# Optimization experiments

Hardware: AMD Instinct MI355X
Metric: run time of the kernel (lower is better)

The kernel has to match this reference:

```python
import jax, jax.numpy as jnp
import numpy as np

B, N, DIM = 2, 2048, 2048
H, KVH, HD = 16, 4, 128
N_REP = H // KVH
SCALE = np.float32(HD ** -0.5)


def setup_inputs() -> dict:
    key = jax.random.key(0)
    ks = jax.random.split(key, 5)
    x = jax.random.normal(ks[0], (B, N, DIM), dtype=jnp.float32)
    mask = jnp.tril(jnp.ones((N, N), dtype=jnp.int32))[None, None]  # [1,1,N,N] causal
    Wq = jax.random.normal(ks[1], (DIM, H * HD), dtype=jnp.float32) * (DIM ** -0.5)
    Wk = jax.random.normal(ks[2], (DIM, KVH * HD), dtype=jnp.float32) * (DIM ** -0.5)
    Wv = jax.random.normal(ks[3], (DIM, KVH * HD), dtype=jnp.float32) * (DIM ** -0.5)
    Wo = jax.random.normal(ks[4], (H * HD, DIM), dtype=jnp.float32) * ((H * HD) ** -0.5)
    return {"x": x, "mask": mask, "Wq": Wq, "Wk": Wk, "Wv": Wv, "Wo": Wo}


def reference(x, mask, Wq, Wk, Wv, Wo):
    Bx, Nx, _ = x.shape
    # projections -> [B, heads, N, head_dim]
    q = (x @ Wq).reshape(Bx, Nx, H, HD).transpose(0, 2, 1, 3)
    k = (x @ Wk).reshape(Bx, Nx, KVH, HD).transpose(0, 2, 1, 3)
    v = (x @ Wv).reshape(Bx, Nx, KVH, HD).transpose(0, 2, 1, 3)
    # repeat_interleave KV heads to match query heads (GQA)
    k = jnp.repeat(k, N_REP, axis=1)
    v = jnp.repeat(v, N_REP, axis=1)
    attn = jnp.einsum('bhqd,bhkd->bhqk', q, k) * SCALE
    attn = jnp.where(mask == 0, jnp.float32(-jnp.inf), attn)
    attn = jax.nn.softmax(attn, axis=-1)
    out = jnp.einsum('bhqk,bhkd->bhqd', attn, v)
    out = out.transpose(0, 2, 1, 3).reshape(Bx, Nx, H * HD)
    return out @ Wo
```

## Files before the change

kernel.cpp:

```cpp
#include <hip/hip_runtime.h>
#include <hip/hip_bf16.h>
#include <math.h>

typedef __bf16 bf16;
typedef bf16 bf16x8 __attribute__((ext_vector_type(8)));
typedef bf16 bf16x4v __attribute__((ext_vector_type(4)));
typedef float f32x4 __attribute__((ext_vector_type(4)));

#define GLD16(g, l) __builtin_amdgcn_global_load_lds(                          \
    (__attribute__((address_space(1))) void*)(g),                              \
    (__attribute__((address_space(3))) void*)(l), 16, 0, 0)

#define MFMA16(a, b, c) __builtin_amdgcn_mfma_f32_16x16x32_bf16((a), (b), (c), 0, 0, 0)

#if __has_builtin(__builtin_amdgcn_exp2f)
#define EXP2F(x) __builtin_amdgcn_exp2f(x)
#else
#define EXP2F(x) exp2f(x)
#endif

__device__ __forceinline__ f32x4 shfl_xor4(f32x4 a, int m) {
  f32x4 r;
  #pragma unroll
  for (int i = 0; i < 4; i++) r[i] = __shfl_xor(a[i], m);
  return r;
}

__global__ void cast_f32_bf16(const float* __restrict__ in, bf16* __restrict__ out, int n4) {
  int i = blockIdx.x * blockDim.x + threadIdx.x;
  if (i < n4) {
    float4 v = ((const float4*)in)[i];
    bf16x4v o;
    o.x = (bf16)v.x; o.y = (bf16)v.y; o.z = (bf16)v.z; o.w = (bf16)v.w;
    ((bf16x4v*)out)[i] = o;
  }
}

__global__ void transpose_cast(const float* __restrict__ in, bf16* __restrict__ out,
                               int colsIn, int outStride, int outRowOff, float scale) {
  __shared__ float t[32][33];
  int c0 = blockIdx.x * 32, r0 = blockIdx.y * 32;
  int tx = threadIdx.x, ty = threadIdx.y;
  #pragma unroll
  for (int i = 0; i < 32; i += 8)
    t[ty + i][tx] = in[(size_t)(r0 + ty + i) * colsIn + (c0 + tx)];
  __syncthreads();
  #pragma unroll
  for (int i = 0; i < 32; i += 8)
    out[(size_t)(outRowOff + c0 + ty + i) * outStride + (r0 + tx)] = (bf16)(t[tx][ty + i] * scale);
}

__global__ void transpose_v(const bf16* __restrict__ QKV, bf16* __restrict__ Vg) {
  __shared__ bf16 t[32][34];
  int n0 = blockIdx.x * 32, d0 = blockIdx.y * 32;
  int bk = blockIdx.z;
  int b = bk >> 2, kvh = bk & 3;
  const bf16* src = QKV + (size_t)b * 2048 * 3072 + 2560 + kvh * 128;
  bf16* dst = Vg + (size_t)bk * 128 * 2048;
  int tx = threadIdx.x, ty = threadIdx.y;
  #pragma unroll
  for (int i = 0; i < 32; i += 8)
    t[ty + i][tx] = src[(size_t)(n0 + ty + i) * 3072 + (d0 + tx)];
  __syncthreads();
  #pragma unroll
  for (int i = 0; i < 32; i += 8)
    dst[(size_t)(d0 + ty + i) * 2048 + (n0 + tx)] = t[tx][ty + i];
}

template <typename OutT>
__global__ __launch_bounds__(256, 2) void gemm_bt(const bf16* __restrict__ A,
                                                  const bf16* __restrict__ Bt,
                                                  OutT* __restrict__ C,
                                                  int M, int N, int K) {
  __shared__ __attribute__((aligned(16))) bf16 As[128 * 32];
  __shared__ __attribute__((aligned(16))) bf16 Bs[128 * 32];
  const int tid = threadIdx.x;
  const int lane = tid & 63;
  const int wave = tid >> 6;
  const int wm = wave >> 1, wn = wave & 1;
  const int l15 = lane & 15, quad = lane >> 4;
  const int rowBase = blockIdx.y * 128;
  const int colBase = blockIdx.x * 128;

  f32x4 acc[4][4] = {};

  const int cb0 = wave * 64;
  const int c0 = cb0 + lane;
  const int c1 = c0 + 256;
  const bf16* a0 = A + (size_t)(rowBase + (c0 >> 2)) * K + (c0 & 3) * 8;
  const bf16* a1 = A + (size_t)(rowBase + (c1 >> 2)) * K + (c1 & 3) * 8;
  const bf16* b0 = Bt + (size_t)(colBase + (c0 >> 2)) * K + (c0 & 3) * 8;
  const bf16* b1 = Bt + (size_t)(colBase + (c1 >> 2)) * K + (c1 & 3) * 8;
  bf16* lA0 = &As[cb0 * 8];
  bf16* lA1 = &As[(cb0 + 256) * 8];
  bf16* lB0 = &Bs[cb0 * 8];
  bf16* lB1 = &Bs[(cb0 + 256) * 8];

  for (int k0 = 0; k0 < K; k0 += 32) {
    GLD16(a0 + k0, lA0);
    GLD16(a1 + k0, lA1);
    GLD16(b0 + k0, lB0);
    GLD16(b1 + k0, lB1);
    __syncthreads();
    bf16x8 af[4], bfr[4];
    #pragma unroll
    for (int i = 0; i < 4; i++)
      af[i] = *(const bf16x8*)&As[(wm * 64 + i * 16 + l15) * 32 + quad * 8];
    #pragma unroll
    for (int i = 0; i < 4; i++)
      bfr[i] = *(const bf16x8*)&Bs[(wn * 64 + i * 16 + l15) * 32 + quad * 8];
    #pragma unroll
    for (int i = 0; i < 4; i++)
      #pragma unroll
      for (int j = 0; j < 4; j++)
        acc[i][j] = MFMA16(af[i], bfr[j], acc[i][j]);
    __syncthreads();
  }

  #pragma unroll
  for (int i = 0; i < 4; i++) {
    int row = rowBase + wm * 64 + i * 16 + quad * 4;
    #pragma unroll
    for (int j = 0; j < 4; j++) {
      int col = colBase + wn * 64 + j * 16 + l15;
      #pragma unroll
      for (int r = 0; r < 4; r++)
        C[(size_t)(row + r) * N + col] = (OutT)acc[i][j][r];
    }
  }
}

#define MASKV (-1e30f)

__global__ __launch_bounds__(256, 2) void gqa_attn(const bf16* __restrict__ QKV,
                                                   const bf16* __restrict__ Vg,
                                                   bf16* __restrict__ Obf) {
  __shared__ __attribute__((aligned(16))) bf16 Kl[64 * 128];
  __shared__ __attribute__((aligned(16))) bf16 Vt[128 * 64];
  __shared__ __attribute__((aligned(16))) bf16 Pl[4][32 * 68];

  const int tid = threadIdx.x;
  const int lane = tid & 63;
  const int wave = tid >> 6;
  const int l15 = lane & 15, quad = lane >> 4;

  int bi = blockIdx.x;
  int bh = bi & 31;
  int jj = (bi & 255) >> 5;
  int qt = (bi < 256) ? (8 + jj) : (7 - jj);
  int b = bh >> 4, h = bh & 15, kvh = h >> 2;
  int q0 = qt * 128;

  const size_t rs = 3072;
  const bf16* Qb  = QKV + (size_t)b * 2048 * rs + h * 128;
  const bf16* Kb  = QKV + (size_t)b * 2048 * rs + 2048 + kvh * 128;
  const bf16* Vgb = Vg + (size_t)(b * 4 + kvh) * 128 * 2048;

  bf16x8 qf[2][4];
  #pragma unroll
  for (int mt = 0; mt < 2; mt++) {
    int row = q0 + wave * 32 + mt * 16 + l15;
    #pragma unroll
    for (int ks = 0; ks < 4; ks++)
      qf[mt][ks] = *(const bf16x8*)&Qb[(size_t)row * rs + ks * 32 + quad * 8];
  }

  const bf16* kp[4]; const bf16* vp[4];
  bf16* kl[4]; bf16* vl[4];
  #pragma unroll
  for (int t = 0; t < 4; t++) {
    int keyl = wave * 16 + t * 4 + (lane >> 4);
    int ck = (lane & 15) ^ (4 * (t & 1) + (lane >> 4));
    kp[t] = Kb + (size_t)keyl * rs + ck * 8;
    kl[t] = &Kl[(wave * 16 + t * 4) * 128];
    int dl = wave * 32 + t * 8 + (lane >> 3);
    int cv = (lane & 7) ^ (lane >> 3);
    vp[t] = Vgb + (size_t)dl * 2048 + cv * 8;
    vl[t] = &Vt[(wave * 32 + t * 8) * 64];
  }

  f32x4 oacc[2][8] = {};
  f32x4 mrow[2], lrow[2];
  #pragma unroll
  for (int mt = 0; mt < 2; mt++)
    #pragma unroll
    for (int r = 0; r < 4; r++) { mrow[mt][r] = MASKV; lrow[mt][r] = 0.f; }

  const int nkt = 2 * qt + 2;
  const int myrow_hi = q0 + wave * 32 + 31;
  for (int kt = 0; kt < nkt; kt++) {
    const int k0 = kt * 64;
    __syncthreads();
    #pragma unroll
    for (int t = 0; t < 4; t++) { GLD16(kp[t], kl[t]); kp[t] += 64 * rs; }
    #pragma unroll
    for (int t = 0; t < 4; t++) { GLD16(vp[t], vl[t]); vp[t] += 64; }
    __syncthreads();

    if (k0 > myrow_hi) continue;

    f32x4 s[2][4] = {};
    #pragma unroll
    for (int ks = 0; ks < 4; ks++) {
      #pragma unroll
      for (int nt = 0; nt < 4; nt++) {
        bf16x8 kf = *(const bf16x8*)&Kl[(nt * 16 + l15) * 128 +
                                        (((ks * 4 + quad) ^ (l15 & 7)) * 8)];
        s[0][nt] = MFMA16(qf[0][ks], kf, s[0][nt]);
        s[1][nt] = MFMA16(qf[1][ks], kf, s[1][nt]);
      }
    }
    if (kt >= nkt - 2) {
      #pragma unroll
      for (int mt = 0; mt < 2; mt++) {
        int rowb = q0 + wave * 32 + mt * 16 + quad * 4;
        #pragma unroll
        for (int nt = 0; nt < 4; nt++) {
          int col = k0 + nt * 16 + l15;
          #pragma unroll
          for (int r = 0; r < 4; r++)
            if (col > rowb + r) s[mt][nt][r] = MASKV;
        }
      }
    }
    #pragma unroll
    for (int mt = 0; mt < 2; mt++) {
      f32x4 mx = s[mt][0];
      #pragma unroll
      for (int nt = 1; nt < 4; nt++)
        #pragma unroll
        for (int r = 0; r < 4; r++) mx[r] = fmaxf(mx[r], s[mt][nt][r]);
      #pragma unroll
      for (int d = 1; d < 16; d <<= 1) {
        f32x4 o = shfl_xor4(mx, d);
        #pragma unroll
        for (int r = 0; r < 4; r++) mx[r] = fmaxf(mx[r], o[r]);
      }
      f32x4 mnew, alpha;
      #pragma unroll
      for (int r = 0; r < 4; r++) {
        mnew[r] = fmaxf(mrow[mt][r], mx[r]);
        alpha[r] = EXP2F(mrow[mt][r] - mnew[r]);
      }
      f32x4 rsum = {0.f, 0.f, 0.f, 0.f};
      #pragma unroll
      for (int nt = 0; nt < 4; nt++)
        #pragma unroll
        for (int r = 0; r < 4; r++) {
          float p = EXP2F(s[mt][nt][r] - mnew[r]);
          s[mt][nt][r] = p;
          rsum[r] += p;
        }
      #pragma unroll
      for (int d = 1; d < 16; d <<= 1) rsum += shfl_xor4(rsum, d);
      #pragma unroll
      for (int r = 0; r < 4; r++) {
        lrow[mt][r] = lrow[mt][r] * alpha[r] + rsum[r];
        mrow[mt][r] = mnew[r];
      }
      #pragma unroll
      for (int no = 0; no < 8; no++)
        #pragma unroll
        for (int r = 0; r < 4; r++) oacc[mt][no][r] *= alpha[r];
      #pragma unroll
      for (int nt = 0; nt < 4; nt++)
        #pragma unroll
        for (int r = 0; r < 4; r++)
          Pl[wave][(mt * 16 + quad * 4 + r) * 68 + nt * 16 + l15] = (bf16)s[mt][nt][r];
    }
    #pragma unroll
    for (int ks2 = 0; ks2 < 2; ks2++) {
      bf16x8 pf0 = *(const bf16x8*)&Pl[wave][l15 * 68 + ks2 * 32 + quad * 8];
      bf16x8 pf1 = *(const bf16x8*)&Pl[wave][(16 + l15) * 68 + ks2 * 32 + quad * 8];
      #pragma unroll
      for (int no = 0; no < 8; no++) {
        bf16x8 vf = *(const bf16x8*)&Vt[(no * 16 + l15) * 64 +
                                        (((ks2 * 4 + quad) ^ (l15 & 7)) * 8)];
        oacc[0][no] = MFMA16(pf0, vf, oacc[0][no]);
        oacc[1][no] = MFMA16(pf1, vf, oacc[1][no]);
      }
    }
  }

  #pragma unroll
  for (int mt = 0; mt < 2; mt++) {
    f32x4 linv;
    #pragma unroll
    for (int r = 0; r < 4; r++) linv[r] = 1.0f / lrow[mt][r];
    int row = q0 + wave * 32 + mt * 16 + quad * 4;
    #pragma unroll
    for (int no = 0; no < 8; no++) {
      int col = h * 128 + no * 16 + l15;
      #pragma unroll
      for (int r = 0; r < 4; r++)
        Obf[(size_t)(b * 2048 + row + r) * 2048 + col] = (bf16)(oacc[mt][no][r] * linv[r]);
    }
  }
}

extern "C" void kernel_launch(void* const* d_in, const int* in_sizes, int n_in,
                              void* d_out, int out_size, void* d_ws, size_t ws_size,
                              hipStream_t stream) {
  const float* x  = (const float*)d_in[0];
  const float* Wq = (const float*)d_in[2];
  const float* Wk = (const float*)d_in[3];
  const float* Wv = (const float*)d_in[4];
  const float* Wo = (const float*)d_in[5];
  float* out = (float*)d_out;

  bf16* Xb    = (bf16*)d_ws;
  bf16* Wqkvt = Xb + 8388608;
  bf16* Wot   = Wqkvt + 6291456;
  bf16* QKV   = Wot + 4194304;
  bf16* Obf   = QKV + 12582912;
  bf16* Vg    = Obf + 8388608;

  const float qscale = (float)(0.08838834764831845 * 1.4426950408889634);

  cast_f32_bf16<<<8192, 256, 0, stream>>>(x, Xb, 2097152);
  dim3 tb(32, 8);
  transpose_cast<<<dim3(64, 64), tb, 0, stream>>>(Wq, Wqkvt, 2048, 2048, 0, qscale);
  transpose_cast<<<dim3(16, 64), tb, 0, stream>>>(Wk, Wqkvt, 512, 2048, 2048, 1.0f);
  transpose_cast<<<dim3(16, 64), tb, 0, stream>>>(Wv, Wqkvt, 512, 2048, 2560, 1.0f);
  transpose_cast<<<dim3(64, 64), tb, 0, stream>>>(Wo, Wot, 2048, 2048, 0, 1.0f);

  gemm_bt<bf16><<<dim3(24, 32), 256, 0, stream>>>(Xb, Wqkvt, QKV, 4096, 3072, 2048);
  transpose_v<<<dim3(64, 4, 8), tb, 0, stream>>>(QKV, Vg);
  gqa_attn<<<512, 256, 0, stream>>>(QKV, Vg, Obf);
  gemm_bt<float><<<dim3(16, 32), 256, 0, stream>>>(Obf, Wot, out, 4096, 2048, 2048);
}
```

Baseline: 339.2 us.

## Double-buffer K/V tiles in LDS and prefetch next tile during compute

After: 349.8 us. 3.1% more time.

```diff
diff --git a/kernel.cpp b/kernel.cpp
--- a/kernel.cpp
+++ b/kernel.cpp
@@ -135,9 +135,9 @@
 __global__ __launch_bounds__(256, 2) void gqa_attn(const bf16* __restrict__ QKV,
                                                    const bf16* __restrict__ Vg,
                                                    bf16* __restrict__ Obf) {
-  __shared__ __attribute__((aligned(16))) bf16 Kl[64 * 128];
-  __shared__ __attribute__((aligned(16))) bf16 Vt[128 * 64];
-  __shared__ __attribute__((aligned(16))) bf16 Pl[4][32 * 68];
+  __shared__ __attribute__((aligned(16))) bf16 Kl[2 * 64 * 128];
+  __shared__ __attribute__((aligned(16))) bf16 Vt[2 * 128 * 64];
+  __shared__ __attribute__((aligned(16))) bf16 Pl[4][16 * 72];
 
   const int tid = threadIdx.x;
   const int lane = tid & 63;
@@ -166,17 +166,17 @@
   }
 
   const bf16* kp[4]; const bf16* vp[4];
-  bf16* kl[4]; bf16* vl[4];
+  int klo[4], vlo[4];
   #pragma unroll
   for (int t = 0; t < 4; t++) {
     int keyl = wave * 16 + t * 4 + (lane >> 4);
     int ck = (lane & 15) ^ (4 * (t & 1) + (lane >> 4));
     kp[t] = Kb + (size_t)keyl * rs + ck * 8;
-    kl[t] = &Kl[(wave * 16 + t * 4) * 128];
+    klo[t] = (wave * 16 + t * 4) * 128;
     int dl = wave * 32 + t * 8 + (lane >> 3);
     int cv = (lane & 7) ^ (lane >> 3);
     vp[t] = Vgb + (size_t)dl * 2048 + cv * 8;
-    vl[t] = &Vt[(wave * 32 + t * 8) * 64];
+    vlo[t] = (wave * 32 + t * 8) * 64;
   }
 
   f32x4 oacc[2][8] = {};
@@ -188,98 +188,119 @@
 
   const int nkt = 2 * qt + 2;
   const int myrow_hi = q0 + wave * 32 + 31;
+
+  #pragma unroll
+  for (int t = 0; t < 4; t++) { GLD16(kp[t], Kl + klo[t]); kp[t] += 64 * rs; }
+  #pragma unroll
+  for (int t = 0; t < 4; t++) { GLD16(vp[t], Vt + vlo[t]); vp[t] += 64; }
+  __syncthreads();
+
   for (int kt = 0; kt < nkt; kt++) {
+    const int cur = kt & 1;
     const int k0 = kt * 64;
-    __syncthreads();
-    #pragma unroll
-    for (int t = 0; t < 4; t++) { GLD16(kp[t], kl[t]); kp[t] += 64 * rs; }
-    #pragma unroll
-    for (int t = 0; t < 4; t++) { GLD16(vp[t], vl[t]); vp[t] += 64; }
-    __syncthreads();
-
-    if (k0 > myrow_hi) continue;
-
-    f32x4 s[2][4] = {};
-    #pragma unroll
-    for (int ks = 0; ks < 4; ks++) {
-      #pragma unroll
-      for (int nt = 0; nt < 4; nt++) {
-        bf16x8 kf = *(const bf16x8*)&Kl[(nt * 16 + l15) * 128 +
-                                        (((ks * 4 + quad) ^ (l15 & 7)) * 8)];
-        s[0][nt] = MFMA16(qf[0][ks], kf, s[0][nt]);
-        s[1][nt] = MFMA16(qf[1][ks], kf, s[1][nt]);
+
+    if (kt + 1 < nkt) {
+      const int nb = (cur ^ 1) * 8192;
+      #pragma unroll
+      for (int t = 0; t < 4; t++) { GLD16(kp[t], Kl + nb + klo[t]); kp[t] += 64 * rs; }
+      #pragma unroll
+      for (int t = 0; t < 4; t++) { GLD16(vp[t], Vt + nb + vlo[t]); vp[t] += 64; }
+    }
+
+    if (k0 <= myrow_hi) {
+      const bf16* Kc = Kl + cur * 8192;
+      const bf16* Vc = Vt + cur * 8192;
+
+      f32x4 s[2][4] = {};
+      __builtin_amdgcn_s_setprio(1);
+      #pragma unroll
+      for (int ks = 0; ks < 4; ks++) {
+        #pragma unroll
+        for (int nt = 0; nt < 4; nt++) {
+          bf16x8 kf = *(const bf16x8*)&Kc[(nt * 16 + l15) * 128 +
+                                          (((ks * 4 + quad) ^ (l15 & 7)) * 8)];
+          s[0][nt] = MFMA16(qf[0][ks], kf, s[0][nt]);
+          s[1][nt] = MFMA16(qf[1][ks], kf, s[1][nt]);
+        }
+      }
+      __builtin_amdgcn_s_setprio(0);
+
+      if (kt >= nkt - 2) {
+        #pragma unroll
+        for (int mt = 0; mt < 2; mt++) {
+          int rowb = q0 + wave * 32 + mt * 16 + quad * 4;
+          #pragma unroll
+          for (int nt = 0; nt < 4; nt++) {
+            int col = k0 + nt * 16 + l15;
+            #pragma unroll
+            for (int r = 0; r < 4; r++)
+              if (col > rowb + r) s[mt][nt][r] = MASKV;
+          }
+        }
+      }
+
+      #pragma unroll
+      for (int mt = 0; mt < 2; mt++) {
+        f32x4 mx = s[mt][0];
+        #pragma unroll
+        for (int nt = 1; nt < 4; nt++)
+          #pragma unroll
+          for (int r = 0; r < 4; r++) mx[r] = fmaxf(mx[r], s[mt][nt][r]);
+        #pragma unroll
+        for (int d = 1; d < 16; d <<= 1) {
+          f32x4 o = shfl_xor4(mx, d);
+          #pragma unroll
+          for (int r = 0; r < 4; r++) mx[r] = fmaxf(mx[r], o[r]);
+        }
+        f32x4 mnew, alpha;
+        #pragma unroll
+        for (int r = 0; r < 4; r++) {
+          mnew[r] = fmaxf(mrow[mt][r], mx[r]);
+          alpha[r] = EXP2F(mrow[mt][r] - mnew[r]);
+        }
+        f32x4 rsum = {0.f, 0.f, 0.f, 0.f};
+        #pragma unroll
+        for (int nt = 0; nt < 4; nt++)
+          #pragma unroll
+          for (int r = 0; r < 4; r++) {
+            float p = EXP2F(s[mt][nt][r] - mnew[r]);
+            s[mt][nt][r] = p;
+            rsum[r] += p;
+          }
+        #pragma unroll
+        for (int d = 1; d < 16; d <<= 1) rsum += shfl_xor4(rsum, d);
+        #pragma unroll
+        for (int r = 0; r < 4; r++) {
+          lrow[mt][r] = lrow[mt][r] * alpha[r] + rsum[r];
+          mrow[mt][r] = mnew[r];
+        }
+        #pragma unroll
+        for (int no = 0; no < 8; no++)
+          #pragma unroll
+          for (int r = 0; r < 4; r++) oacc[mt][no][r] *= alpha[r];
+
+        #pragma unroll
+        for (int nt = 0; nt < 4; nt++)
+          #pragma unroll
+          for (int r = 0; r < 4; r++)
+            Pl[wave][(quad * 4 + r) * 72 + nt * 16 + l15] = (bf16)s[mt][nt][r];
+
+        __builtin_amdgcn_s_setprio(1);
+        #pragma unroll
+        for (int ks2 = 0; ks2 < 2; ks2++) {
+          bf16x8 pf = *(const bf16x8*)&Pl[wave][l15 * 72 + ks2 * 32 + quad * 8];
+          #pragma unroll
+          for (int no = 0; no < 8; no++) {
+            bf16x8 vf = *(const bf16x8*)&Vc[(no * 16 + l15) * 64 +
+                                            (((ks2 * 4 + quad) ^ (l15 & 7)) * 8)];
+            oacc[mt][no] = MFMA16(pf, vf, oacc[mt][no]);
+          }
+        }
+        __builtin_amdgcn_s_setprio(0);
       }
     }
-    if (kt >= nkt - 2) {
-      #pragma unroll
-      for (int mt = 0; mt < 2; mt++) {
-        int rowb = q0 + wave * 32 + mt * 16 + quad * 4;
-        #pragma unroll
-        for (int nt = 0; nt < 4; nt++) {
-          int col = k0 + nt * 16 + l15;
-          #pragma unroll
-          for (int r = 0; r < 4; r++)
-            if (col > rowb + r) s[mt][nt][r] = MASKV;
-        }
-      }
-    }
-    #pragma unroll
-    for (int mt = 0; mt < 2; mt++) {
-      f32x4 mx = s[mt][0];
-      #pragma unroll
-      for (int nt = 1; nt < 4; nt++)
-        #pragma unroll
-        for (int r = 0; r < 4; r++) mx[r] = fmaxf(mx[r], s[mt][nt][r]);
-      #pragma unroll
-      for (int d = 1; d < 16; d <<= 1) {
-        f32x4 o = shfl_xor4(mx, d);
-        #pragma unroll
-        for (int r = 0; r < 4; r++) mx[r] = fmaxf(mx[r], o[r]);
-      }
-      f32x4 mnew, alpha;
-      #pragma unroll
-      for (int r = 0; r < 4; r++) {
-        mnew[r] = fmaxf(mrow[mt][r], mx[r]);
-        alpha[r] = EXP2F(mrow[mt][r] - mnew[r]);
-      }
-      f32x4 rsum = {0.f, 0.f, 0.f, 0.f};
-      #pragma unroll
-      for (int nt = 0; nt < 4; nt++)
-        #pragma unroll
-        for (int r = 0; r < 4; r++) {
-          float p = EXP2F(s[mt][nt][r] - mnew[r]);
-          s[mt][nt][r] = p;
-          rsum[r] += p;
-        }
-      #pragma unroll
-      for (int d = 1; d < 16; d <<= 1) rsum += shfl_xor4(rsum, d);
-      #pragma unroll
-      for (int r = 0; r < 4; r++) {
-        lrow[mt][r] = lrow[mt][r] * alpha[r] + rsum[r];
-        mrow[mt][r] = mnew[r];
-      }
-      #pragma unroll
-      for (int no = 0; no < 8; no++)
-        #pragma unroll
-        for (int r = 0; r < 4; r++) oacc[mt][no][r] *= alpha[r];
-      #pragma unroll
-      for (int nt = 0; nt < 4; nt++)
-        #pragma unroll
-        for (int r = 0; r < 4; r++)
-          Pl[wave][(mt * 16 + quad * 4 + r) * 68 + nt * 16 + l15] = (bf16)s[mt][nt][r];
-    }
-    #pragma unroll
-    for (int ks2 = 0; ks2 < 2; ks2++) {
-      bf16x8 pf0 = *(const bf16x8*)&Pl[wave][l15 * 68 + ks2 * 32 + quad * 8];
-      bf16x8 pf1 = *(const bf16x8*)&Pl[wave][(16 + l15) * 68 + ks2 * 32 + quad * 8];
-      #pragma unroll
-      for (int no = 0; no < 8; no++) {
-        bf16x8 vf = *(const bf16x8*)&Vt[(no * 16 + l15) * 64 +
-                                        (((ks2 * 4 + quad) ^ (l15 & 7)) * 8)];
-        oacc[0][no] = MFMA16(pf0, vf, oacc[0][no]);
-        oacc[1][no] = MFMA16(pf1, vf, oacc[1][no]);
-      }
-    }
+
+    __syncthreads();
   }
 
   #pragma unroll
```

## Split KV range of longest causal query tiles across two blocks with merge kernel

Applied to the files above, without the earlier changes.

Result: no change. 337.0 us (-0.6%).

```diff
diff --git a/kernel.cpp b/kernel.cpp
--- a/kernel.cpp
+++ b/kernel.cpp
@@ -132,9 +132,18 @@
 
 #define MASKV (-1e30f)
 
+__device__ const unsigned char BMAP[22] = {
+  28, 58, 24, 50, 20, 46, 36, 32,
+  62, 59, 54, 51, 47, 42, 55, 63,
+  0, 4, 8, 12, 16, 43
+};
+
+#define SLOT_F32 16640
+
 __global__ __launch_bounds__(256, 2) void gqa_attn(const bf16* __restrict__ QKV,
                                                    const bf16* __restrict__ Vg,
-                                                   bf16* __restrict__ Obf) {
+                                                   bf16* __restrict__ Obf,
+                                                   float* __restrict__ Part) {
   __shared__ __attribute__((aligned(16))) bf16 Kl[64 * 128];
   __shared__ __attribute__((aligned(16))) bf16 Vt[128 * 64];
   __shared__ __attribute__((aligned(16))) bf16 Pl[4][32 * 68];
@@ -144,12 +153,16 @@
   const int wave = tid >> 6;
   const int l15 = lane & 15, quad = lane >> 4;
 
-  int bi = blockIdx.x;
-  int bh = bi & 31;
-  int jj = (bi & 255) >> 5;
-  int qt = (bi < 256) ? (8 + jj) : (7 - jj);
-  int b = bh >> 4, h = bh & 15, kvh = h >> 2;
-  int q0 = qt * 128;
+  const int e = BMAP[blockIdx.x >> 5];
+  const int bh = blockIdx.x & 31;
+  const int qt = e >> 2;
+  const int split = (e >> 1) & 1;
+  const int half = e & 1;
+  const int b = bh >> 4, h = bh & 15, kvh = h >> 2;
+  const int q0 = qt * 128;
+  const int nkt = 2 * qt + 2;
+  const int kt_lo = (split && half) ? (nkt >> 1) : 0;
+  const int kt_hi = (split && !half) ? (nkt >> 1) : nkt;
 
   const size_t rs = 3072;
   const bf16* Qb  = QKV + (size_t)b * 2048 * rs + h * 128;
@@ -171,11 +184,11 @@
   for (int t = 0; t < 4; t++) {
     int keyl = wave * 16 + t * 4 + (lane >> 4);
     int ck = (lane & 15) ^ (4 * (t & 1) + (lane >> 4));
-    kp[t] = Kb + (size_t)keyl * rs + ck * 8;
+    kp[t] = Kb + (size_t)(kt_lo * 64 + keyl) * rs + ck * 8;
     kl[t] = &Kl[(wave * 16 + t * 4) * 128];
     int dl = wave * 32 + t * 8 + (lane >> 3);
     int cv = (lane & 7) ^ (lane >> 3);
-    vp[t] = Vgb + (size_t)dl * 2048 + cv * 8;
+    vp[t] = Vgb + (size_t)dl * 2048 + kt_lo * 64 + cv * 8;
     vl[t] = &Vt[(wave * 32 + t * 8) * 64];
   }
 
@@ -186,9 +199,8 @@
     #pragma unroll
     for (int r = 0; r < 4; r++) { mrow[mt][r] = MASKV; lrow[mt][r] = 0.f; }
 
-  const int nkt = 2 * qt + 2;
   const int myrow_hi = q0 + wave * 32 + 31;
-  for (int kt = 0; kt < nkt; kt++) {
+  for (int kt = kt_lo; kt < kt_hi; kt++) {
     const int k0 = kt * 64;
     __syncthreads();
     #pragma unroll
@@ -282,19 +294,72 @@
     }
   }
 
-  #pragma unroll
-  for (int mt = 0; mt < 2; mt++) {
-    f32x4 linv;
-    #pragma unroll
-    for (int r = 0; r < 4; r++) linv[r] = 1.0f / lrow[mt][r];
-    int row = q0 + wave * 32 + mt * 16 + quad * 4;
-    #pragma unroll
-    for (int no = 0; no < 8; no++) {
-      int col = h * 128 + no * 16 + l15;
-      #pragma unroll
-      for (int r = 0; r < 4; r++)
-        Obf[(size_t)(b * 2048 + row + r) * 2048 + col] = (bf16)(oacc[mt][no][r] * linv[r]);
-    }
+  if (!split) {
+    #pragma unroll
+    for (int mt = 0; mt < 2; mt++) {
+      f32x4 linv;
+      #pragma unroll
+      for (int r = 0; r < 4; r++) linv[r] = 1.0f / lrow[mt][r];
+      int row = q0 + wave * 32 + mt * 16 + quad * 4;
+      #pragma unroll
+      for (int no = 0; no < 8; no++) {
+        int col = h * 128 + no * 16 + l15;
+        #pragma unroll
+        for (int r = 0; r < 4; r++)
+          Obf[(size_t)(b * 2048 + row + r) * 2048 + col] = (bf16)(oacc[mt][no][r] * linv[r]);
+      }
+    }
+  } else {
+    const int fidx = bh * 6 + (qt - 10);
+    float* slot = Part + (size_t)(fidx * 2 + half) * SLOT_F32;
+    #pragma unroll
+    for (int mt = 0; mt < 2; mt++) {
+      int row = wave * 32 + mt * 16 + quad * 4;
+      #pragma unroll
+      for (int no = 0; no < 8; no++) {
+        int col = no * 16 + l15;
+        #pragma unroll
+        for (int r = 0; r < 4; r++)
+          slot[(row + r) * 128 + col] = oacc[mt][no][r];
+      }
+    }
+    if (l15 == 0) {
+      #pragma unroll
+      for (int mt = 0; mt < 2; mt++)
+        #pragma unroll
+        for (int r = 0; r < 4; r++) {
+          int row = wave * 32 + mt * 16 + quad * 4 + r;
+          slot[16384 + row] = mrow[mt][r];
+          slot[16512 + row] = lrow[mt][r];
+        }
+    }
+  }
+}
+
+__global__ __launch_bounds__(256) void merge_split(const float* __restrict__ Part,
+                                                   bf16* __restrict__ Obf) {
+  const int fidx = blockIdx.x;
+  const int bh = fidx / 6, qt = 10 + fidx % 6;
+  const int b = bh >> 4, h = bh & 15;
+  const int tid = threadIdx.x;
+  const int cl = (tid & 31) * 4;
+  const int r0 = tid >> 5;
+  const float* s0 = Part + (size_t)(fidx * 2) * SLOT_F32;
+  const float* s1 = s0 + SLOT_F32;
+  #pragma unroll
+  for (int i = 0; i < 16; i++) {
+    int row = r0 + i * 8;
+    float m0 = s0[16384 + row], l0 = s0[16512 + row];
+    float m1 = s1[16384 + row], l1 = s1[16512 + row];
+    float ms = fmaxf(m0, m1);
+    float a0 = EXP2F(m0 - ms), a1 = EXP2F(m1 - ms);
+    float linv = 1.0f / (l0 * a0 + l1 * a1);
+    f32x4 v0 = *(const f32x4*)&s0[row * 128 + cl];
+    f32x4 v1 = *(const f32x4*)&s1[row * 128 + cl];
+    bf16x4v o;
+    #pragma unroll
+    for (int r = 0; r < 4; r++) o[r] = (bf16)((v0[r] * a0 + v1[r] * a1) * linv);
+    *(bf16x4v*)&Obf[(size_t)(b * 2048 + qt * 128 + row) * 2048 + h * 128 + cl] = o;
   }
 }
 
@@ -315,6 +380,8 @@
   bf16* Obf   = QKV + 12582912;
   bf16* Vg    = Obf + 8388608;
 
+  float* Part = (float*)d_ws;
+
   const float qscale = (float)(0.08838834764831845 * 1.4426950408889634);
 
   cast_f32_bf16<<<8192, 256, 0, stream>>>(x, Xb, 2097152);
@@ -326,6 +393,7 @@
 
   gemm_bt<bf16><<<dim3(24, 32), 256, 0, stream>>>(Xb, Wqkvt, QKV, 4096, 3072, 2048);
   transpose_v<<<dim3(64, 4, 8), tb, 0, stream>>>(QKV, Vg);
-  gqa_attn<<<512, 256, 0, stream>>>(QKV, Vg, Obf);
+  gqa_attn<<<704, 256, 0, stream>>>(QKV, Vg, Obf, Part);
+  merge_split<<<192, 256, 0, stream>>>(Part, Obf);
   gemm_bt<float><<<dim3(16, 32), 256, 0, stream>>>(Obf, Wot, out, 4096, 2048, 2048);
 }
```
